# Kernel optimization log

Measured on AMD Instinct MI355X. Metric: run time of the kernel, lower is better.

The kernel has to match this reference:

```python
import math
import jax, jax.numpy as jnp
import numpy as np

D_MODEL = 2048
NUM_EXPERTS = 64
Z_LOSS_COEF = 1e-3
AUX_LOSS_COEF = 1e-2
CAPACITY_FACTOR = 1.0
MIN_CAPACITY = 4


def setup_inputs() -> dict:
    key = jax.random.key(0)
    kx, kw = jax.random.split(key)
    x = jax.random.normal(kx, (4, 4096, D_MODEL), dtype=jnp.float32)
    W = 0.02 * jax.random.normal(kw, (NUM_EXPERTS, D_MODEL), dtype=jnp.float32)  # gate weight [E, D]
    return {"x": x, "W": W}


def reference(x, W):
    B, T, D = x.shape
    N = B * T                      # num_tokens
    E = W.shape[0]
    x_flat = x.reshape(N, D)

    logits = jnp.einsum("nd,ed->ne", x_flat, W)          # gate GEMM [N, E]
    probs = jax.nn.softmax(logits, axis=-1)

    # z-loss: mean(logsumexp(logits)^2)
    z_loss = jnp.mean(jnp.square(jax.nn.logsumexp(logits, axis=-1)))

    expert_index = jnp.argmax(logits, axis=-1)            # [N] int
    expert_prob = jnp.take_along_axis(probs, expert_index[:, None], axis=-1)[:, 0]  # [N]

    counts = jnp.bincount(expert_index, length=E)         # [E] int
    f_i = counts.astype(probs.dtype) / N                  # fraction routed per expert
    p_i = jnp.mean(probs, axis=0)                         # mean router prob per expert
    aux_loss = AUX_LOSS_COEF * E * jnp.sum(f_i * p_i) + Z_LOSS_COEF * z_loss

    capacity = max(MIN_CAPACITY, math.ceil(CAPACITY_FACTOR * N / E))  # static int
    return expert_index, expert_prob, counts, capacity, aux_loss
```

## Files before the change

kernel.cpp:

```cpp
#include <hip/hip_runtime.h>
#include <math.h>

#define D_MODEL 2048
#define NE      64
#define TB      64
#define KS      2
#define KSEG    (D_MODEL / KS)
#define KC      128
#define NCH     (KSEG / KC)
#define FB_KC   32
#define FB_NCH  (D_MODEL / FB_KC)

typedef _Float16 half8 __attribute__((ext_vector_type(8)));
typedef float    f32x4 __attribute__((ext_vector_type(4)));

#define CVT1(F, HV, LV, J) do {                                               \
    float _f = (F);                                                           \
    _Float16 _h = (_Float16)_f;                                               \
    HV[J] = _h;                                                               \
    LV[J] = (_Float16)(_f - (float)_h);                                       \
} while (0)

__global__ __launch_bounds__(256) void wcvt_kernel(
    const float* __restrict__ W, short* __restrict__ Wh, short* __restrict__ Wl)
{
    const int e = blockIdx.x, t = threadIdx.x, c = t * 8;
    const float* src = W + (size_t)e * D_MODEL + c;
    float4 v0 = *(const float4*)src;
    float4 v1 = *(const float4*)(src + 4);
    half8 hv, lv;
    CVT1(v0.x * 64.0f, hv, lv, 0); CVT1(v0.y * 64.0f, hv, lv, 1);
    CVT1(v0.z * 64.0f, hv, lv, 2); CVT1(v0.w * 64.0f, hv, lv, 3);
    CVT1(v1.x * 64.0f, hv, lv, 4); CVT1(v1.y * 64.0f, hv, lv, 5);
    CVT1(v1.z * 64.0f, hv, lv, 6); CVT1(v1.w * 64.0f, hv, lv, 7);
    *(half8*)(Wh + (size_t)e * D_MODEL + c) = hv;
    *(half8*)(Wl + (size_t)e * D_MODEL + c) = lv;
}

__global__ __launch_bounds__(256, 2) void router_mfma(
    const float* __restrict__ x, const short* __restrict__ Whg,
    const short* __restrict__ Wlg, float* __restrict__ part, int ntiles)
{
    __shared__ __align__(16) char smem[65536];
    _Float16* Ah = (_Float16*)smem;
    _Float16* Al = (_Float16*)(smem + 16384);
    _Float16* Wh = (_Float16*)(smem + 32768);
    _Float16* Wl = (_Float16*)(smem + 49152);

    const int t    = threadIdx.x;
    const int tile = blockIdx.x;
    const int ks   = blockIdx.y;
    const int m0   = tile * TB;
    const int k0   = ks * KSEG;
    const int l    = t & 63;
    const int wv   = t >> 6;

    const int srow = t >> 4;
    const int sslt = t & 15;
    const int soff0 = ((sslt ^ (srow & 7)) << 3);

    float4 pa0, pa1, pa2, pa3, pa4, pa5, pa6, pa7;
    uint4  pwh0, pwh1, pwh2, pwh3, pwl0, pwl1, pwl2, pwl3;

#define PREFETCH(KB) do {                                                     \
    const float* _ap0 = x + (size_t)(m0 +  0 + srow) * D_MODEL + (KB) + sslt * 8; \
    const float* _ap1 = x + (size_t)(m0 + 16 + srow) * D_MODEL + (KB) + sslt * 8; \
    const float* _ap2 = x + (size_t)(m0 + 32 + srow) * D_MODEL + (KB) + sslt * 8; \
    const float* _ap3 = x + (size_t)(m0 + 48 + srow) * D_MODEL + (KB) + sslt * 8; \
    pa0 = *(const float4*)_ap0; pa1 = *(const float4*)(_ap0 + 4);             \
    pa2 = *(const float4*)_ap1; pa3 = *(const float4*)(_ap1 + 4);             \
    pa4 = *(const float4*)_ap2; pa5 = *(const float4*)(_ap2 + 4);             \
    pa6 = *(const float4*)_ap3; pa7 = *(const float4*)(_ap3 + 4);             \
    const size_t _w0 = (size_t)( 0 + srow) * D_MODEL + (KB) + sslt * 8;       \
    const size_t _w1 = (size_t)(16 + srow) * D_MODEL + (KB) + sslt * 8;       \
    const size_t _w2 = (size_t)(32 + srow) * D_MODEL + (KB) + sslt * 8;       \
    const size_t _w3 = (size_t)(48 + srow) * D_MODEL + (KB) + sslt * 8;       \
    pwh0 = *(const uint4*)&Whg[_w0]; pwh1 = *(const uint4*)&Whg[_w1];         \
    pwh2 = *(const uint4*)&Whg[_w2]; pwh3 = *(const uint4*)&Whg[_w3];         \
    pwl0 = *(const uint4*)&Wlg[_w0]; pwl1 = *(const uint4*)&Wlg[_w1];         \
    pwl2 = *(const uint4*)&Wlg[_w2]; pwl3 = *(const uint4*)&Wlg[_w3];         \
} while (0)

#define STORE_ITEM(I, PA, PB, PWH, PWL) do {                                  \
    half8 _hv, _lv;                                                           \
    CVT1((PA).x * 8.0f, _hv, _lv, 0); CVT1((PA).y * 8.0f, _hv, _lv, 1);       \
    CVT1((PA).z * 8.0f, _hv, _lv, 2); CVT1((PA).w * 8.0f, _hv, _lv, 3);       \
    CVT1((PB).x * 8.0f, _hv, _lv, 4); CVT1((PB).y * 8.0f, _hv, _lv, 5);       \
    CVT1((PB).z * 8.0f, _hv, _lv, 6); CVT1((PB).w * 8.0f, _hv, _lv, 7);       \
    const int _off = ((I) * 16 + srow) * 128 + soff0;                         \
    *(half8*)&Ah[_off] = _hv;                                                 \
    *(half8*)&Al[_off] = _lv;                                                 \
    *(uint4*)&Wh[_off] = PWH;                                                 \
    *(uint4*)&Wl[_off] = PWL;                                                 \
} while (0)

    PREFETCH(k0);

    f32x4 acc0 = {0.f,0.f,0.f,0.f}, acc1 = {0.f,0.f,0.f,0.f};
    f32x4 acc2 = {0.f,0.f,0.f,0.f}, acc3 = {0.f,0.f,0.f,0.f};

    for (int ch = 0; ch < NCH; ++ch) {
        __builtin_amdgcn_s_barrier();
        STORE_ITEM(0, pa0, pa1, pwh0, pwl0);
        STORE_ITEM(1, pa2, pa3, pwh1, pwl1);
        STORE_ITEM(2, pa4, pa5, pwh2, pwl2);
        STORE_ITEM(3, pa6, pa7, pwh3, pwl3);
        __builtin_amdgcn_s_barrier();
        if (ch + 1 < NCH)
            PREFETCH(k0 + (ch + 1) * KC);

        const int arow = wv * 16 + (l & 15);
        const int rsw  = l & 7;
        #pragma unroll
        for (int kq = 0; kq < 4; ++kq) {
            const int s    = kq * 4 + (l >> 4);
            const int aoff = arow * 128 + ((s ^ rsw) << 3);
            half8 ah = *(const half8*)&Ah[aoff];
            half8 al = *(const half8*)&Al[aoff];
            #pragma unroll
            for (int n = 0; n < 4; ++n) {
                const int woff = (n * 16 + (l & 15)) * 128 + ((s ^ rsw) << 3);
                half8 wh = *(const half8*)&Wh[woff];
                half8 wl = *(const half8*)&Wl[woff];
                f32x4 a = (n == 0) ? acc0 : (n == 1) ? acc1 : (n == 2) ? acc2 : acc3;
                a = __builtin_amdgcn_mfma_f32_16x16x32_f16(al, wl, a, 0, 0, 0);
                a = __builtin_amdgcn_mfma_f32_16x16x32_f16(al, wh, a, 0, 0, 0);
                a = __builtin_amdgcn_mfma_f32_16x16x32_f16(ah, wl, a, 0, 0, 0);
                a = __builtin_amdgcn_mfma_f32_16x16x32_f16(ah, wh, a, 0, 0, 0);
                if (n == 0) acc0 = a; else if (n == 1) acc1 = a;
                else if (n == 2) acc2 = a; else acc3 = a;
            }
        }
    }

    float* dst = part + ((size_t)tile * KS + ks) * (TB * NE);
    const int rbase = wv * 16 + (l >> 4) * 4;
    const int col0  = l & 15;
    #pragma unroll
    for (int q = 0; q < 4; ++q) {
        dst[(rbase + q) * NE +  0 + col0] = acc0[q] * (1.0f / 512.0f);
        dst[(rbase + q) * NE + 16 + col0] = acc1[q] * (1.0f / 512.0f);
        dst[(rbase + q) * NE + 32 + col0] = acc2[q] * (1.0f / 512.0f);
        dst[(rbase + q) * NE + 48 + col0] = acc3[q] * (1.0f / 512.0f);
    }
}

__global__ __launch_bounds__(1024) void router_stats5(
    const float* __restrict__ part, float* __restrict__ out,
    float* __restrict__ ws_prob, float* __restrict__ ws_z,
    int* __restrict__ ws_cnt, int Ntok)
{
    __shared__ float sL[64][NE + 1];
    __shared__ float red16[64][16];
    __shared__ int   arg16[64][16];
    __shared__ float smax[64], sinv[64];
    __shared__ float spart[16][NE];
    __shared__ int   hist[NE];

    const int t = threadIdx.x, b = blockIdx.x, m0 = b * 64;
    const float* base = part + (size_t)b * KS * (TB * NE);

    {
        const float* p0 = base + (size_t)t * 4;
        float s0 = 0.f, s1 = 0.f, s2 = 0.f, s3 = 0.f;
        #pragma unroll
        for (int j = 0; j < KS; ++j) {
            float4 v = *(const float4*)(p0 + (size_t)j * (TB * NE));
            s0 += v.x; s1 += v.y; s2 += v.z; s3 += v.w;
        }
        const int row = t >> 4, col = (t & 15) << 2;
        sL[row][col]     = s0; sL[row][col + 1] = s1;
        sL[row][col + 2] = s2; sL[row][col + 3] = s3;
    }
    if (t < NE) hist[t] = 0;
    __syncthreads();

    {
        const int m = t >> 4, qr = t & 15;
        float mx = -3.4e38f; int ag = qr * 4;
        #pragma unroll
        for (int k = 0; k < 4; ++k) {
            const int e = qr * 4 + k;
            float v = sL[m][e];
            if (v > mx) { mx = v; ag = e; }
        }
        red16[m][qr] = mx; arg16[m][qr] = ag;
    }
    __syncthreads();
    if (t < 64) {
        const int m = t;
        float mx = red16[m][0]; int ag = arg16[m][0];
        #pragma unroll
        for (int qr = 1; qr < 16; ++qr)
            if (red16[m][qr] > mx) { mx = red16[m][qr]; ag = arg16[m][qr]; }
        smax[m] = mx;
        out[m0 + m] = (float)ag;
        atomicAdd(&hist[ag], 1);
    }
    __syncthreads();
    {
        const int m = t >> 4, qr = t & 15;
        const float mx = smax[m];
        float s = 0.f;
        #pragma unroll
        for (int k = 0; k < 4; ++k) s += expf(sL[m][qr * 4 + k] - mx);
        red16[m][qr] = s;
    }
    __syncthreads();
    if (t < 64) {
        const int m = t;
        float s = 0.f;
        #pragma unroll
        for (int qr = 0; qr < 16; ++qr) s += red16[m][qr];
        float inv = 1.f / s;
        sinv[m] = inv;
        out[Ntok + m0 + m] = inv;
        float lse = smax[m] + logf(s);
        float z = lse * lse;
        #pragma unroll
        for (int off = 32; off > 0; off >>= 1) z += __shfl_down(z, off, 64);
        if (t == 0) ws_z[b] = z;
    }
    __syncthreads();
    {
        const int e = t & 63, g = t >> 6;
        float pa = 0.f;
        #pragma unroll
        for (int k = 0; k < 4; ++k) {
            const int m = g * 4 + k;
            pa += expf(sL[m][e] - smax[m]) * sinv[m];
        }
        spart[g][e] = pa;
    }
    __syncthreads();
    if (t < NE) {
        float ps = 0.f;
        #pragma unroll
        for (int g = 0; g < 16; ++g) ps += spart[g][t];
        ws_prob[b * NE + t] = ps;
        ws_cnt[b * NE + t]  = hist[t];
    }
}

__global__ __launch_bounds__(256) void router_final2(
    const float* __restrict__ ws_prob, const float* __restrict__ ws_z,
    const int* __restrict__ ws_cnt, float* __restrict__ out,
    int Ntok, int nblocks)
{
    __shared__ float sp[4][NE];
    __shared__ int   sc[4][NE];
    __shared__ float sz[4];

    const int e = threadIdx.x & 63, g = threadIdx.x >> 6;
    const int per = nblocks / 4;
    const int hi  = (g == 3) ? nblocks : (g + 1) * per;

    float ps = 0.f; int c = 0;
    for (int blk = g * per; blk < hi; ++blk) {
        ps += ws_prob[blk * NE + e];
        c  += ws_cnt[blk * NE + e];
    }
    sp[g][e] = ps; sc[g][e] = c;

    float z = 0.f;
    for (int blk = (int)threadIdx.x; blk < nblocks; blk += 256) z += ws_z[blk];
    #pragma unroll
    for (int off = 32; off > 0; off >>= 1) z += __shfl_down(z, off, 64);
    if (e == 0) sz[g] = z;
    __syncthreads();

    if (threadIdx.x < 64) {
        const int ee = threadIdx.x;
        float pst = ((sp[0][ee] + sp[1][ee]) + sp[2][ee]) + sp[3][ee];
        int   ct  = ((sc[0][ee] + sc[1][ee]) + sc[2][ee]) + sc[3][ee];
        out[2 * Ntok + ee] = (float)ct;

        float fN = (float)Ntok;
        float fp = ((float)ct / fN) * (pst / fN);
        #pragma unroll
        for (int off = 32; off > 0; off >>= 1) fp += __shfl_down(fp, off, 64);
        if (ee == 0) {
            float zt = ((sz[0] + sz[1]) + sz[2]) + sz[3];
            int cap = (Ntok + NE - 1) / NE;
            if (cap < 4) cap = 4;
            float aux = 0.01f * (float)NE * fp + 1e-3f * (zt / fN);
            out[2 * Ntok + NE]     = (float)cap;
            out[2 * Ntok + NE + 1] = aux;
        }
    }
}

__global__ __launch_bounds__(256) void router_main_fb(
    const float* __restrict__ x, const float* __restrict__ W,
    float* __restrict__ out, float* __restrict__ ws_prob,
    float* __restrict__ ws_z, int* __restrict__ ws_cnt, int Ntok)
{
    __shared__ __align__(16) float sX[FB_KC][68];
    __shared__ __align__(16) float sW[FB_KC][68];
    __shared__ float sL[64][65];
    __shared__ float smax[64], sinv[64];
    __shared__ float spart[4][NE];
    __shared__ int   hist[NE];

    const int t = threadIdx.x, b = blockIdx.x, m0 = b * 64;
    const int mq = t & 15, nq = t >> 4;
    const int r1 = t >> 3, r2 = r1 + 32, c1 = (t & 7) << 2;
    const float* xp1 = x + (size_t)(m0 + r1) * D_MODEL + c1;
    const float* xp2 = x + (size_t)(m0 + r2) * D_MODEL + c1;
    const float* wp1 = W + (size_t)r1 * D_MODEL + c1;
    const float* wp2 = W + (size_t)r2 * D_MODEL + c1;
    float4 ax1 = *(const float4*)xp1, ax2 = *(const float4*)xp2;
    float4 aw1 = *(const float4*)wp1, aw2 = *(const float4*)wp2;
    float a1[4][4] = {}, a2[4][4] = {};
    for (int ch = 0; ch < FB_NCH; ++ch) {
        __syncthreads();
        sX[c1+0][r1] = ax1.x; sX[c1+1][r1] = ax1.y; sX[c1+2][r1] = ax1.z; sX[c1+3][r1] = ax1.w;
        sX[c1+0][r2] = ax2.x; sX[c1+1][r2] = ax2.y; sX[c1+2][r2] = ax2.z; sX[c1+3][r2] = ax2.w;
        sW[c1+0][r1] = aw1.x; sW[c1+1][r1] = aw1.y; sW[c1+2][r1] = aw1.z; sW[c1+3][r1] = aw1.w;
        sW[c1+0][r2] = aw2.x; sW[c1+1][r2] = aw2.y; sW[c1+2][r2] = aw2.z; sW[c1+3][r2] = aw2.w;
        __syncthreads();
        if (ch + 1 < FB_NCH) {
            xp1 += FB_KC; xp2 += FB_KC; wp1 += FB_KC; wp2 += FB_KC;
            ax1 = *(const float4*)xp1; ax2 = *(const float4*)xp2;
            aw1 = *(const float4*)wp1; aw2 = *(const float4*)wp2;
        }
        #pragma unroll
        for (int k = 0; k < FB_KC; ++k) {
            float4 xa = *(const float4*)&sX[k][mq << 2];
            float4 wb = *(const float4*)&sW[k][nq << 2];
            float (*A)[4] = (k < FB_KC / 2) ? a1 : a2;
            A[0][0] = fmaf(xa.x, wb.x, A[0][0]); A[0][1] = fmaf(xa.x, wb.y, A[0][1]);
            A[0][2] = fmaf(xa.x, wb.z, A[0][2]); A[0][3] = fmaf(xa.x, wb.w, A[0][3]);
            A[1][0] = fmaf(xa.y, wb.x, A[1][0]); A[1][1] = fmaf(xa.y, wb.y, A[1][1]);
            A[1][2] = fmaf(xa.y, wb.z, A[1][2]); A[1][3] = fmaf(xa.y, wb.w, A[1][3]);
            A[2][0] = fmaf(xa.z, wb.x, A[2][0]); A[2][1] = fmaf(xa.z, wb.y, A[2][1]);
            A[2][2] = fmaf(xa.z, wb.z, A[2][2]); A[2][3] = fmaf(xa.z, wb.w, A[2][3]);
            A[3][0] = fmaf(xa.w, wb.x, A[3][0]); A[3][1] = fmaf(xa.w, wb.y, A[3][1]);
            A[3][2] = fmaf(xa.w, wb.z, A[3][2]); A[3][3] = fmaf(xa.w, wb.w, A[3][3]);
        }
    }
    #pragma unroll
    for (int i = 0; i < 4; ++i)
        #pragma unroll
        for (int j = 0; j < 4; ++j)
            sL[(mq << 2) + i][(nq << 2) + j] = a1[i][j] + a2[i][j];
    if (t < NE) hist[t] = 0;
    __syncthreads();
    if (t < 64) {
        const int m = t;
        float mx = sL[m][0]; int arg = 0;
        for (int e = 1; e < NE; ++e) { float v = sL[m][e]; if (v > mx) { mx = v; arg = e; } }
        float s = 0.f;
        for (int e = 0; e < NE; ++e) s += expf(sL[m][e] - mx);
        float inv = 1.f / s;
        out[m0 + m] = (float)arg; out[Ntok + m0 + m] = inv;
        smax[m] = mx; sinv[m] = inv;
        atomicAdd(&hist[arg], 1);
        float lse = mx + logf(s); float z = lse * lse;
        for (int off = 32; off > 0; off >>= 1) z += __shfl_down(z, off, 64);
        if (t == 0) ws_z[b] = z;
    }
    __syncthreads();
    {
        const int e = t & 63, mg = t >> 6;
        float pa = 0.f;
        for (int m = mg * 16; m < mg * 16 + 16; ++m) pa += expf(sL[m][e] - smax[m]) * sinv[m];
        spart[mg][e] = pa;
    }
    __syncthreads();
    if (t < NE) {
        ws_prob[b * NE + t] = spart[0][t] + spart[1][t] + spart[2][t] + spart[3][t];
        ws_cnt[b * NE + t]  = hist[t];
    }
}

extern "C" void kernel_launch(void* const* d_in, const int* in_sizes, int n_in,
                              void* d_out, int out_size, void* d_ws, size_t ws_size,
                              hipStream_t stream)
{
    const float* x = (const float*)d_in[0];
    const float* W = (const float*)d_in[1];
    float* out = (float*)d_out;

    const int Ntok   = in_sizes[0] / D_MODEL;
    const int ntiles = Ntok / TB;
    const int nstat  = Ntok / 64;

    const size_t wh_elems   = (size_t)NE * D_MODEL;
    const size_t part_elems = (size_t)ntiles * KS * TB * NE;
    const size_t need = wh_elems * 2 * 2
                      + (part_elems + (size_t)nstat * NE + nstat) * 4
                      + (size_t)nstat * NE * 4 + 1024;

    if ((Ntok % TB) == 0 && ws_size >= need) {
        short* wsh    = (short*)d_ws;
        short* wsl    = wsh + wh_elems;
        float* ws_part = (float*)(wsl + wh_elems);
        float* ws_prob = ws_part + part_elems;
        float* ws_z    = ws_prob + (size_t)nstat * NE;
        int*   ws_cnt  = (int*)(ws_z + nstat);

        wcvt_kernel<<<NE, 256, 0, stream>>>(W, wsh, wsl);
        dim3 grid(ntiles, KS);
        router_mfma<<<grid, 256, 0, stream>>>(x, wsh, wsl, ws_part, ntiles);
        router_stats5<<<nstat, 1024, 0, stream>>>(ws_part, out, ws_prob, ws_z, ws_cnt, Ntok);
        router_final2<<<1, 256, 0, stream>>>(ws_prob, ws_z, ws_cnt, out, Ntok, nstat);
    } else {
        const int nb = Ntok / 64;
        float* ws_prob = (float*)d_ws;
        float* ws_z    = ws_prob + (size_t)nb * NE;
        int*   ws_cnt  = (int*)(ws_z + nb);
        router_main_fb<<<nb, 256, 0, stream>>>(x, W, out, ws_prob, ws_z, ws_cnt, Ntok);
        router_final2<<<1, 256, 0, stream>>>(ws_prob, ws_z, ws_cnt, out, Ntok, nb);
    }
}
```

Baseline: 61.60 us.

## Fuse router GEMM with softmax stats and drop the K-split

Merges the MFMA gate GEMM and the per-token softmax/argmax/histogram kernel into one kernel. Each block now owns the full K range for its 64 tokens, so partial sums no longer round-trip through global memory. The x prefetch becomes double-buffered in registers, one tile ahead, to hide load latency. In exchange the grid halves (256 blocks instead of 512), which lowers parallelism across CUs, and register pressure rises from the extra prefetch buffers.

After: 64.63 us. 1.05x slower.

```diff
diff --git a/kernel.cpp b/kernel.cpp
--- a/kernel.cpp
+++ b/kernel.cpp
@@ -4,10 +4,8 @@
 #define D_MODEL 2048
 #define NE      64
 #define TB      64
-#define KS      2
-#define KSEG    (D_MODEL / KS)
 #define KC      128
-#define NCH     (KSEG / KC)
+#define NCH     (D_MODEL / KC)
 #define FB_KC   32
 #define FB_NCH  (D_MODEL / FB_KC)
 
@@ -37,40 +35,51 @@
     *(half8*)(Wl + (size_t)e * D_MODEL + c) = lv;
 }
 
-__global__ __launch_bounds__(256, 2) void router_mfma(
+__global__ __launch_bounds__(256, 2) void router_fused(
     const float* __restrict__ x, const short* __restrict__ Whg,
-    const short* __restrict__ Wlg, float* __restrict__ part, int ntiles)
+    const short* __restrict__ Wlg, float* __restrict__ out,
+    float* __restrict__ ws_prob, float* __restrict__ ws_z,
+    int* __restrict__ ws_cnt, int Ntok)
 {
     __shared__ __align__(16) char smem[65536];
     _Float16* Ah = (_Float16*)smem;
     _Float16* Al = (_Float16*)(smem + 16384);
     _Float16* Wh = (_Float16*)(smem + 32768);
     _Float16* Wl = (_Float16*)(smem + 49152);
-
-    const int t    = threadIdx.x;
-    const int tile = blockIdx.x;
-    const int ks   = blockIdx.y;
-    const int m0   = tile * TB;
-    const int k0   = ks * KSEG;
-    const int l    = t & 63;
-    const int wv   = t >> 6;
-
-    const int srow = t >> 4;
-    const int sslt = t & 15;
+    float (*sL)[NE + 1] = (float (*)[NE + 1])smem;
+    float (*red4)[4]    = (float (*)[4])(smem + 20480);
+    int   (*arg4)[4]    = (int (*)[4])(smem + 24576);
+    float* smax         = (float*)(smem + 28672);
+    float* sinv         = (float*)(smem + 28928);
+    float (*spart)[NE]  = (float (*)[NE])(smem + 29184);
+    int*   hist         = (int*)(smem + 30720);
+
+    const int t  = threadIdx.x;
+    const int b  = blockIdx.x;
+    const int m0 = b * TB;
+    const int l  = t & 63;
+    const int wv = t >> 6;
+
+    const int srow  = t >> 4;
+    const int sslt  = t & 15;
     const int soff0 = ((sslt ^ (srow & 7)) << 3);
 
-    float4 pa0, pa1, pa2, pa3, pa4, pa5, pa6, pa7;
+    float4 paA0, paA1, paA2, paA3, paA4, paA5, paA6, paA7;
+    float4 paB0, paB1, paB2, paB3, paB4, paB5, paB6, paB7;
     uint4  pwh0, pwh1, pwh2, pwh3, pwl0, pwl1, pwl2, pwl3;
 
-#define PREFETCH(KB) do {                                                     \
-    const float* _ap0 = x + (size_t)(m0 +  0 + srow) * D_MODEL + (KB) + sslt * 8; \
-    const float* _ap1 = x + (size_t)(m0 + 16 + srow) * D_MODEL + (KB) + sslt * 8; \
-    const float* _ap2 = x + (size_t)(m0 + 32 + srow) * D_MODEL + (KB) + sslt * 8; \
-    const float* _ap3 = x + (size_t)(m0 + 48 + srow) * D_MODEL + (KB) + sslt * 8; \
-    pa0 = *(const float4*)_ap0; pa1 = *(const float4*)(_ap0 + 4);             \
-    pa2 = *(const float4*)_ap1; pa3 = *(const float4*)(_ap1 + 4);             \
-    pa4 = *(const float4*)_ap2; pa5 = *(const float4*)(_ap2 + 4);             \
-    pa6 = *(const float4*)_ap3; pa7 = *(const float4*)(_ap3 + 4);             \
+#define PRE_A(P0, P1, P2, P3, P4, P5, P6, P7, KB) do {                        \
+    const float* _a0 = x + (size_t)(m0 +  0 + srow) * D_MODEL + (KB) + sslt * 8; \
+    const float* _a1 = x + (size_t)(m0 + 16 + srow) * D_MODEL + (KB) + sslt * 8; \
+    const float* _a2 = x + (size_t)(m0 + 32 + srow) * D_MODEL + (KB) + sslt * 8; \
+    const float* _a3 = x + (size_t)(m0 + 48 + srow) * D_MODEL + (KB) + sslt * 8; \
+    P0 = *(const float4*)_a0; P1 = *(const float4*)(_a0 + 4);                 \
+    P2 = *(const float4*)_a1; P3 = *(const float4*)(_a1 + 4);                 \
+    P4 = *(const float4*)_a2; P5 = *(const float4*)(_a2 + 4);                 \
+    P6 = *(const float4*)_a3; P7 = *(const float4*)(_a3 + 4);                 \
+} while (0)
+
+#define PRE_W(KB) do {                                                        \
     const size_t _w0 = (size_t)( 0 + srow) * D_MODEL + (KB) + sslt * 8;       \
     const size_t _w1 = (size_t)(16 + srow) * D_MODEL + (KB) + sslt * 8;       \
     const size_t _w2 = (size_t)(32 + srow) * D_MODEL + (KB) + sslt * 8;       \
@@ -94,124 +103,114 @@
     *(uint4*)&Wl[_off] = PWL;                                                 \
 } while (0)
 
-    PREFETCH(k0);
+#define STORE_SET(P0, P1, P2, P3, P4, P5, P6, P7) do {                        \
+    STORE_ITEM(0, P0, P1, pwh0, pwl0);                                        \
+    STORE_ITEM(1, P2, P3, pwh1, pwl1);                                        \
+    STORE_ITEM(2, P4, P5, pwh2, pwl2);                                        \
+    STORE_ITEM(3, P6, P7, pwh3, pwl3);                                        \
+} while (0)
+
+#define MFMA_PHASE() do {                                                     \
+    const int arow = wv * 16 + (l & 15);                                      \
+    const int rsw  = l & 7;                                                   \
+    _Pragma("unroll")                                                         \
+    for (int kq = 0; kq < 4; ++kq) {                                          \
+        const int s    = kq * 4 + (l >> 4);                                   \
+        const int aoff = arow * 128 + ((s ^ rsw) << 3);                       \
+        half8 ah = *(const half8*)&Ah[aoff];                                  \
+        half8 al = *(const half8*)&Al[aoff];                                  \
+        _Pragma("unroll")                                                     \
+        for (int n = 0; n < 4; ++n) {                                         \
+            const int woff = (n * 16 + (l & 15)) * 128 + ((s ^ rsw) << 3);    \
+            half8 wh = *(const half8*)&Wh[woff];                              \
+            half8 wl = *(const half8*)&Wl[woff];                              \
+            f32x4 a = (n == 0) ? acc0 : (n == 1) ? acc1 : (n == 2) ? acc2 : acc3; \
+            a = __builtin_amdgcn_mfma_f32_16x16x32_f16(al, wl, a, 0, 0, 0);   \
+            a = __builtin_amdgcn_mfma_f32_16x16x32_f16(al, wh, a, 0, 0, 0);   \
+            a = __builtin_amdgcn_mfma_f32_16x16x32_f16(ah, wl, a, 0, 0, 0);   \
+            a = __builtin_amdgcn_mfma_f32_16x16x32_f16(ah, wh, a, 0, 0, 0);   \
+            if (n == 0) acc0 = a; else if (n == 1) acc1 = a;                  \
+            else if (n == 2) acc2 = a; else acc3 = a;                         \
+        }                                                                     \
+    }                                                                         \
+} while (0)
 
     f32x4 acc0 = {0.f,0.f,0.f,0.f}, acc1 = {0.f,0.f,0.f,0.f};
     f32x4 acc2 = {0.f,0.f,0.f,0.f}, acc3 = {0.f,0.f,0.f,0.f};
 
-    for (int ch = 0; ch < NCH; ++ch) {
+    PRE_A(paA0, paA1, paA2, paA3, paA4, paA5, paA6, paA7, 0);
+    PRE_W(0);
+    PRE_A(paB0, paB1, paB2, paB3, paB4, paB5, paB6, paB7, KC);
+
+    for (int ch = 0; ch < NCH; ch += 2) {
         __builtin_amdgcn_s_barrier();
-        STORE_ITEM(0, pa0, pa1, pwh0, pwl0);
-        STORE_ITEM(1, pa2, pa3, pwh1, pwl1);
-        STORE_ITEM(2, pa4, pa5, pwh2, pwl2);
-        STORE_ITEM(3, pa6, pa7, pwh3, pwl3);
+        STORE_SET(paA0, paA1, paA2, paA3, paA4, paA5, paA6, paA7);
+        asm volatile("s_waitcnt lgkmcnt(0)" ::: "memory");
         __builtin_amdgcn_s_barrier();
-        if (ch + 1 < NCH)
-            PREFETCH(k0 + (ch + 1) * KC);
-
-        const int arow = wv * 16 + (l & 15);
-        const int rsw  = l & 7;
-        #pragma unroll
-        for (int kq = 0; kq < 4; ++kq) {
-            const int s    = kq * 4 + (l >> 4);
-            const int aoff = arow * 128 + ((s ^ rsw) << 3);
-            half8 ah = *(const half8*)&Ah[aoff];
-            half8 al = *(const half8*)&Al[aoff];
-            #pragma unroll
-            for (int n = 0; n < 4; ++n) {
-                const int woff = (n * 16 + (l & 15)) * 128 + ((s ^ rsw) << 3);
-                half8 wh = *(const half8*)&Wh[woff];
-                half8 wl = *(const half8*)&Wl[woff];
-                f32x4 a = (n == 0) ? acc0 : (n == 1) ? acc1 : (n == 2) ? acc2 : acc3;
-                a = __builtin_amdgcn_mfma_f32_16x16x32_f16(al, wl, a, 0, 0, 0);
-                a = __builtin_amdgcn_mfma_f32_16x16x32_f16(al, wh, a, 0, 0, 0);
-                a = __builtin_amdgcn_mfma_f32_16x16x32_f16(ah, wl, a, 0, 0, 0);
-                a = __builtin_amdgcn_mfma_f32_16x16x32_f16(ah, wh, a, 0, 0, 0);
-                if (n == 0) acc0 = a; else if (n == 1) acc1 = a;
-                else if (n == 2) acc2 = a; else acc3 = a;
-            }
-        }
-    }
-
-    float* dst = part + ((size_t)tile * KS + ks) * (TB * NE);
-    const int rbase = wv * 16 + (l >> 4) * 4;
-    const int col0  = l & 15;
-    #pragma unroll
-    for (int q = 0; q < 4; ++q) {
-        dst[(rbase + q) * NE +  0 + col0] = acc0[q] * (1.0f / 512.0f);
-        dst[(rbase + q) * NE + 16 + col0] = acc1[q] * (1.0f / 512.0f);
-        dst[(rbase + q) * NE + 32 + col0] = acc2[q] * (1.0f / 512.0f);
-        dst[(rbase + q) * NE + 48 + col0] = acc3[q] * (1.0f / 512.0f);
-    }
-}
-
-__global__ __launch_bounds__(1024) void router_stats5(
-    const float* __restrict__ part, float* __restrict__ out,
-    float* __restrict__ ws_prob, float* __restrict__ ws_z,
-    int* __restrict__ ws_cnt, int Ntok)
-{
-    __shared__ float sL[64][NE + 1];
-    __shared__ float red16[64][16];
-    __shared__ int   arg16[64][16];
-    __shared__ float smax[64], sinv[64];
-    __shared__ float spart[16][NE];
-    __shared__ int   hist[NE];
-
-    const int t = threadIdx.x, b = blockIdx.x, m0 = b * 64;
-    const float* base = part + (size_t)b * KS * (TB * NE);
-
+        if (ch + 1 < NCH) PRE_W((ch + 1) * KC);
+        if (ch + 2 < NCH)
+            PRE_A(paA0, paA1, paA2, paA3, paA4, paA5, paA6, paA7, (ch + 2) * KC);
+        MFMA_PHASE();
+        __builtin_amdgcn_s_barrier();
+        STORE_SET(paB0, paB1, paB2, paB3, paB4, paB5, paB6, paB7);
+        asm volatile("s_waitcnt lgkmcnt(0)" ::: "memory");
+        __builtin_amdgcn_s_barrier();
+        if (ch + 2 < NCH) PRE_W((ch + 2) * KC);
+        if (ch + 3 < NCH)
+            PRE_A(paB0, paB1, paB2, paB3, paB4, paB5, paB6, paB7, (ch + 3) * KC);
+        MFMA_PHASE();
+    }
+
+    __syncthreads();
     {
-        const float* p0 = base + (size_t)t * 4;
-        float s0 = 0.f, s1 = 0.f, s2 = 0.f, s3 = 0.f;
-        #pragma unroll
-        for (int j = 0; j < KS; ++j) {
-            float4 v = *(const float4*)(p0 + (size_t)j * (TB * NE));
-            s0 += v.x; s1 += v.y; s2 += v.z; s3 += v.w;
-        }
-        const int row = t >> 4, col = (t & 15) << 2;
-        sL[row][col]     = s0; sL[row][col + 1] = s1;
-        sL[row][col + 2] = s2; sL[row][col + 3] = s3;
+        const int rbase = wv * 16 + (l >> 4) * 4;
+        const int col0  = l & 15;
+        #pragma unroll
+        for (int q = 0; q < 4; ++q) {
+            sL[rbase + q][ 0 + col0] = acc0[q] * (1.0f / 512.0f);
+            sL[rbase + q][16 + col0] = acc1[q] * (1.0f / 512.0f);
+            sL[rbase + q][32 + col0] = acc2[q] * (1.0f / 512.0f);
+            sL[rbase + q][48 + col0] = acc3[q] * (1.0f / 512.0f);
+        }
     }
     if (t < NE) hist[t] = 0;
     __syncthreads();
 
     {
-        const int m = t >> 4, qr = t & 15;
-        float mx = -3.4e38f; int ag = qr * 4;
-        #pragma unroll
-        for (int k = 0; k < 4; ++k) {
-            const int e = qr * 4 + k;
+        const int m = t >> 2, qr = t & 3;
+        float mx = -3.4e38f; int ag = 0;
+        #pragma unroll
+        for (int k = 0; k < 16; ++k) {
+            const int e = qr * 16 + k;
             float v = sL[m][e];
             if (v > mx) { mx = v; ag = e; }
         }
-        red16[m][qr] = mx; arg16[m][qr] = ag;
+        red4[m][qr] = mx; arg4[m][qr] = ag;
     }
     __syncthreads();
     if (t < 64) {
         const int m = t;
-        float mx = red16[m][0]; int ag = arg16[m][0];
-        #pragma unroll
-        for (int qr = 1; qr < 16; ++qr)
-            if (red16[m][qr] > mx) { mx = red16[m][qr]; ag = arg16[m][qr]; }
+        float mx = red4[m][0]; int ag = arg4[m][0];
+        #pragma unroll
+        for (int qr = 1; qr < 4; ++qr)
+            if (red4[m][qr] > mx) { mx = red4[m][qr]; ag = arg4[m][qr]; }
         smax[m] = mx;
         out[m0 + m] = (float)ag;
         atomicAdd(&hist[ag], 1);
     }
     __syncthreads();
     {
-        const int m = t >> 4, qr = t & 15;
+        const int m = t >> 2, qr = t & 3;
         const float mx = smax[m];
         float s = 0.f;
         #pragma unroll
-        for (int k = 0; k < 4; ++k) s += expf(sL[m][qr * 4 + k] - mx);
-        red16[m][qr] = s;
+        for (int k = 0; k < 16; ++k) s += expf(sL[m][qr * 16 + k] - mx);
+        red4[m][qr] = s;
     }
     __syncthreads();
     if (t < 64) {
         const int m = t;
-        float s = 0.f;
-        #pragma unroll
-        for (int qr = 0; qr < 16; ++qr) s += red16[m][qr];
+        float s = ((red4[m][0] + red4[m][1]) + red4[m][2]) + red4[m][3];
         float inv = 1.f / s;
         sinv[m] = inv;
         out[Ntok + m0 + m] = inv;
@@ -223,21 +222,18 @@
     }
     __syncthreads();
     {
-        const int e = t & 63, g = t >> 6;
+        const int e = t & 63, mg = t >> 6;
         float pa = 0.f;
         #pragma unroll
-        for (int k = 0; k < 4; ++k) {
-            const int m = g * 4 + k;
+        for (int k = 0; k < 16; ++k) {
+            const int m = mg * 16 + k;
             pa += expf(sL[m][e] - smax[m]) * sinv[m];
         }
-        spart[g][e] = pa;
+        spart[mg][e] = pa;
     }
     __syncthreads();
     if (t < NE) {
-        float ps = 0.f;
-        #pragma unroll
-        for (int g = 0; g < 16; ++g) ps += spart[g][t];
-        ws_prob[b * NE + t] = ps;
+        ws_prob[b * NE + t] = ((spart[0][t] + spart[1][t]) + spart[2][t]) + spart[3][t];
         ws_cnt[b * NE + t]  = hist[t];
     }
 }
@@ -382,29 +378,25 @@
     const float* W = (const float*)d_in[1];
     float* out = (float*)d_out;
 
-    const int Ntok   = in_sizes[0] / D_MODEL;
-    const int ntiles = Ntok / TB;
-    const int nstat  = Ntok / 64;
-
-    const size_t wh_elems   = (size_t)NE * D_MODEL;
-    const size_t part_elems = (size_t)ntiles * KS * TB * NE;
+    const int Ntok = in_sizes[0] / D_MODEL;
+    const int nblk = Ntok / TB;
+
+    const size_t wh_elems = (size_t)NE * D_MODEL;
     const size_t need = wh_elems * 2 * 2
-                      + (part_elems + (size_t)nstat * NE + nstat) * 4
-                      + (size_t)nstat * NE * 4 + 1024;
-
-    if ((Ntok % TB) == 0 && ws_size >= need) {
-        short* wsh    = (short*)d_ws;
-        short* wsl    = wsh + wh_elems;
-        float* ws_part = (float*)(wsl + wh_elems);
-        float* ws_prob = ws_part + part_elems;
-        float* ws_z    = ws_prob + (size_t)nstat * NE;
-        int*   ws_cnt  = (int*)(ws_z + nstat);
+                      + ((size_t)nblk * NE + nblk) * 4
+                      + (size_t)nblk * NE * 4 + 1024;
+
+    if ((Ntok % TB) == 0 && (nblk % 4) == 0 && ws_size >= need) {
+        short* wsh     = (short*)d_ws;
+        short* wsl     = wsh + wh_elems;
+        float* ws_prob = (float*)(wsl + wh_elems);
+        float* ws_z    = ws_prob + (size_t)nblk * NE;
+        int*   ws_cnt  = (int*)(ws_z + nblk);
 
         wcvt_kernel<<<NE, 256, 0, stream>>>(W, wsh, wsl);
-        dim3 grid(ntiles, KS);
-        router_mfma<<<grid, 256, 0, stream>>>(x, wsh, wsl, ws_part, ntiles);
-        router_stats5<<<nstat, 1024, 0, stream>>>(ws_part, out, ws_prob, ws_z, ws_cnt, Ntok);
-        router_final2<<<1, 256, 0, stream>>>(ws_prob, ws_z, ws_cnt, out, Ntok, nstat);
+        router_fused<<<nblk, 256, 0, stream>>>(x, wsh, wsl, out,
+                                               ws_prob, ws_z, ws_cnt, Ntok);
+        router_final2<<<1, 256, 0, stream>>>(ws_prob, ws_z, ws_cnt, out, Ntok, nblk);
     } else {
         const int nb = Ntok / 64;
         float* ws_prob = (float*)d_ws;
```

## Load activations straight to registers and double-buffer weights in LDS

Applied to the files above, without the earlier changes.

The gate GEMM kernel is restructured so activations are loaded from global memory directly into registers in MFMA fragment layout and split into fp16 hi/lo there, instead of being staged through shared memory. Only the weight hi/lo tiles go through a double-buffered 32KB LDS region. The K chunk shrinks to 64 and each wave computes a 2x2 block of 16x16 tiles. This is meant to cut LDS traffic and barrier stalls and to overlap global loads with MFMA work, at the cost of more register pressure and less coalesced per-lane loads of x.

New measurement: 72.80 us. 18.2% more time.

```diff
diff --git a/kernel.cpp b/kernel.cpp
--- a/kernel.cpp
+++ b/kernel.cpp
@@ -4,10 +4,9 @@
 #define D_MODEL 2048
 #define NE      64
 #define TB      64
-#define KS      2
-#define KSEG    (D_MODEL / KS)
-#define KC      128
-#define NCH     (KSEG / KC)
+#define KHALF   1024
+#define KC      64
+#define NCH     (KHALF / KC)
 #define FB_KC   32
 #define FB_NCH  (D_MODEL / FB_KC)
 
@@ -37,111 +36,144 @@
     *(half8*)(Wl + (size_t)e * D_MODEL + c) = lv;
 }
 
-__global__ __launch_bounds__(256, 2) void router_mfma(
+__global__ __launch_bounds__(256, 2) void router_gemm_v4(
     const float* __restrict__ x, const short* __restrict__ Whg,
     const short* __restrict__ Wlg, float* __restrict__ part, int ntiles)
 {
-    __shared__ __align__(16) char smem[65536];
-    _Float16* Ah = (_Float16*)smem;
-    _Float16* Al = (_Float16*)(smem + 16384);
-    _Float16* Wh = (_Float16*)(smem + 32768);
-    _Float16* Wl = (_Float16*)(smem + 49152);
+    __shared__ __align__(16) char smem[32768];
 
     const int t    = threadIdx.x;
     const int tile = blockIdx.x;
     const int ks   = blockIdx.y;
     const int m0   = tile * TB;
-    const int k0   = ks * KSEG;
+    const int k0   = ks * KHALF;
     const int l    = t & 63;
     const int wv   = t >> 6;
-
-    const int srow = t >> 4;
-    const int sslt = t & 15;
-    const int soff0 = ((sslt ^ (srow & 7)) << 3);
-
-    float4 pa0, pa1, pa2, pa3, pa4, pa5, pa6, pa7;
-    uint4  pwh0, pwh1, pwh2, pwh3, pwl0, pwl1, pwl2, pwl3;
-
-#define PREFETCH(KB) do {                                                     \
-    const float* _ap0 = x + (size_t)(m0 +  0 + srow) * D_MODEL + (KB) + sslt * 8; \
-    const float* _ap1 = x + (size_t)(m0 + 16 + srow) * D_MODEL + (KB) + sslt * 8; \
-    const float* _ap2 = x + (size_t)(m0 + 32 + srow) * D_MODEL + (KB) + sslt * 8; \
-    const float* _ap3 = x + (size_t)(m0 + 48 + srow) * D_MODEL + (KB) + sslt * 8; \
-    pa0 = *(const float4*)_ap0; pa1 = *(const float4*)(_ap0 + 4);             \
-    pa2 = *(const float4*)_ap1; pa3 = *(const float4*)(_ap1 + 4);             \
-    pa4 = *(const float4*)_ap2; pa5 = *(const float4*)(_ap2 + 4);             \
-    pa6 = *(const float4*)_ap3; pa7 = *(const float4*)(_ap3 + 4);             \
-    const size_t _w0 = (size_t)( 0 + srow) * D_MODEL + (KB) + sslt * 8;       \
-    const size_t _w1 = (size_t)(16 + srow) * D_MODEL + (KB) + sslt * 8;       \
-    const size_t _w2 = (size_t)(32 + srow) * D_MODEL + (KB) + sslt * 8;       \
-    const size_t _w3 = (size_t)(48 + srow) * D_MODEL + (KB) + sslt * 8;       \
-    pwh0 = *(const uint4*)&Whg[_w0]; pwh1 = *(const uint4*)&Whg[_w1];         \
-    pwh2 = *(const uint4*)&Whg[_w2]; pwh3 = *(const uint4*)&Whg[_w3];         \
-    pwl0 = *(const uint4*)&Wlg[_w0]; pwl1 = *(const uint4*)&Wlg[_w1];         \
-    pwl2 = *(const uint4*)&Wlg[_w2]; pwl3 = *(const uint4*)&Wlg[_w3];         \
+    const int mp   = wv & 1;
+    const int np   = wv >> 1;
+
+    const int srow = t >> 2;
+    const int sc   = t & 3;
+    const int ssw  = srow & 7;
+    const int sof0 = (srow << 6) + (((sc * 2 + 0) ^ ssw) << 3);
+    const int sof1 = (srow << 6) + (((sc * 2 + 1) ^ ssw) << 3);
+    const size_t wsrc = (size_t)srow * D_MODEL + k0 + sc * 16;
+
+    const int koff = (l >> 4) * 8;
+    const float* abase0 = x + (size_t)(m0 + mp * 32 +  0 + (l & 15)) * D_MODEL + k0 + koff;
+    const float* abase1 = x + (size_t)(m0 + mp * 32 + 16 + (l & 15)) * D_MODEL + k0 + koff;
+
+    f32x4 a00 = {0.f,0.f,0.f,0.f}, a01 = {0.f,0.f,0.f,0.f};
+    f32x4 a10 = {0.f,0.f,0.f,0.f}, a11 = {0.f,0.f,0.f,0.f};
+
+    uint4  whA0, whA1, wlA0, wlA1;
+    uint4  whB0, whB1, wlB0, wlB1;
+    float4 e00, e01, e02, e03, e10, e11, e12, e13;
+    float4 o00, o01, o02, o03, o10, o11, o12, o13;
+
+#define PRE_W(WH0, WH1, WL0, WL1, CH) do {                                    \
+    const size_t _o = wsrc + (size_t)(CH) * KC;                               \
+    WH0 = *(const uint4*)&Whg[_o];     WH1 = *(const uint4*)&Whg[_o + 8];     \
+    WL0 = *(const uint4*)&Wlg[_o];     WL1 = *(const uint4*)&Wlg[_o + 8];     \
 } while (0)
 
-#define STORE_ITEM(I, PA, PB, PWH, PWL) do {                                  \
-    half8 _hv, _lv;                                                           \
-    CVT1((PA).x * 8.0f, _hv, _lv, 0); CVT1((PA).y * 8.0f, _hv, _lv, 1);       \
-    CVT1((PA).z * 8.0f, _hv, _lv, 2); CVT1((PA).w * 8.0f, _hv, _lv, 3);       \
-    CVT1((PB).x * 8.0f, _hv, _lv, 4); CVT1((PB).y * 8.0f, _hv, _lv, 5);       \
-    CVT1((PB).z * 8.0f, _hv, _lv, 6); CVT1((PB).w * 8.0f, _hv, _lv, 7);       \
-    const int _off = ((I) * 16 + srow) * 128 + soff0;                         \
-    *(half8*)&Ah[_off] = _hv;                                                 \
-    *(half8*)&Al[_off] = _lv;                                                 \
-    *(uint4*)&Wh[_off] = PWH;                                                 \
-    *(uint4*)&Wl[_off] = PWL;                                                 \
+#define STORE_W(WH0, WH1, WL0, WL1, BB) do {                                  \
+    _Float16* _Wh = (_Float16*)(smem + (BB) * 16384);                         \
+    _Float16* _Wl = (_Float16*)(smem + (BB) * 16384 + 8192);                  \
+    *(uint4*)&_Wh[sof0] = WH0;  *(uint4*)&_Wh[sof1] = WH1;                    \
+    *(uint4*)&_Wl[sof0] = WL0;  *(uint4*)&_Wl[sof1] = WL1;                    \
 } while (0)
 
-    PREFETCH(k0);
-
-    f32x4 acc0 = {0.f,0.f,0.f,0.f}, acc1 = {0.f,0.f,0.f,0.f};
-    f32x4 acc2 = {0.f,0.f,0.f,0.f}, acc3 = {0.f,0.f,0.f,0.f};
-
-    for (int ch = 0; ch < NCH; ++ch) {
+#define PRE_A(P00, P01, P02, P03, P10, P11, P12, P13, CH) do {                \
+    const float* _b0 = abase0 + (size_t)(CH) * KC;                            \
+    const float* _b1 = abase1 + (size_t)(CH) * KC;                            \
+    P00 = *(const float4*)_b0;        P01 = *(const float4*)(_b0 + 4);        \
+    P02 = *(const float4*)(_b0 + 32); P03 = *(const float4*)(_b0 + 36);       \
+    P10 = *(const float4*)_b1;        P11 = *(const float4*)(_b1 + 4);        \
+    P12 = *(const float4*)(_b1 + 32); P13 = *(const float4*)(_b1 + 36);       \
+} while (0)
+
+#define MFMA_PHASE(BB, P00, P01, P02, P03, P10, P11, P12, P13) do {           \
+    const _Float16* _Wh = (const _Float16*)(smem + (BB) * 16384);             \
+    const _Float16* _Wl = (const _Float16*)(smem + (BB) * 16384 + 8192);      \
+    _Pragma("unroll")                                                         \
+    for (int kq = 0; kq < 2; ++kq) {                                          \
+        half8 ah0, al0, ah1, al1;                                             \
+        if (kq == 0) {                                                        \
+            CVT1((P00).x * 8.0f, ah0, al0, 0); CVT1((P00).y * 8.0f, ah0, al0, 1); \
+            CVT1((P00).z * 8.0f, ah0, al0, 2); CVT1((P00).w * 8.0f, ah0, al0, 3); \
+            CVT1((P01).x * 8.0f, ah0, al0, 4); CVT1((P01).y * 8.0f, ah0, al0, 5); \
+            CVT1((P01).z * 8.0f, ah0, al0, 6); CVT1((P01).w * 8.0f, ah0, al0, 7); \
+            CVT1((P10).x * 8.0f, ah1, al1, 0); CVT1((P10).y * 8.0f, ah1, al1, 1); \
+            CVT1((P10).z * 8.0f, ah1, al1, 2); CVT1((P10).w * 8.0f, ah1, al1, 3); \
+            CVT1((P11).x * 8.0f, ah1, al1, 4); CVT1((P11).y * 8.0f, ah1, al1, 5); \
+            CVT1((P11).z * 8.0f, ah1, al1, 6); CVT1((P11).w * 8.0f, ah1, al1, 7); \
+        } else {                                                              \
+            CVT1((P02).x * 8.0f, ah0, al0, 0); CVT1((P02).y * 8.0f, ah0, al0, 1); \
+            CVT1((P02).z * 8.0f, ah0, al0, 2); CVT1((P02).w * 8.0f, ah0, al0, 3); \
+            CVT1((P03).x * 8.0f, ah0, al0, 4); CVT1((P03).y * 8.0f, ah0, al0, 5); \
+            CVT1((P03).z * 8.0f, ah0, al0, 6); CVT1((P03).w * 8.0f, ah0, al0, 7); \
+            CVT1((P12).x * 8.0f, ah1, al1, 0); CVT1((P12).y * 8.0f, ah1, al1, 1); \
+            CVT1((P12).z * 8.0f, ah1, al1, 2); CVT1((P12).w * 8.0f, ah1, al1, 3); \
+            CVT1((P13).x * 8.0f, ah1, al1, 4); CVT1((P13).y * 8.0f, ah1, al1, 5); \
+            CVT1((P13).z * 8.0f, ah1, al1, 6); CVT1((P13).w * 8.0f, ah1, al1, 7); \
+        }                                                                     \
+        const int _s = kq * 4 + (l >> 4);                                     \
+        _Pragma("unroll")                                                     \
+        for (int n = 0; n < 2; ++n) {                                         \
+            const int _row  = np * 32 + n * 16 + (l & 15);                    \
+            const int _woff = (_row << 6) + (((_s ^ (_row & 7))) << 3);       \
+            half8 _wh = *(const half8*)&_Wh[_woff];                           \
+            half8 _wl = *(const half8*)&_Wl[_woff];                           \
+            f32x4 _a = (n == 0) ? a00 : a01;                                  \
+            _a = __builtin_amdgcn_mfma_f32_16x16x32_f16(al0, _wl, _a, 0, 0, 0); \
+            _a = __builtin_amdgcn_mfma_f32_16x16x32_f16(al0, _wh, _a, 0, 0, 0); \
+            _a = __builtin_amdgcn_mfma_f32_16x16x32_f16(ah0, _wl, _a, 0, 0, 0); \
+            _a = __builtin_amdgcn_mfma_f32_16x16x32_f16(ah0, _wh, _a, 0, 0, 0); \
+            if (n == 0) a00 = _a; else a01 = _a;                              \
+            f32x4 _b = (n == 0) ? a10 : a11;                                  \
+            _b = __builtin_amdgcn_mfma_f32_16x16x32_f16(al1, _wl, _b, 0, 0, 0); \
+            _b = __builtin_amdgcn_mfma_f32_16x16x32_f16(al1, _wh, _b, 0, 0, 0); \
+            _b = __builtin_amdgcn_mfma_f32_16x16x32_f16(ah1, _wl, _b, 0, 0, 0); \
+            _b = __builtin_amdgcn_mfma_f32_16x16x32_f16(ah1, _wh, _b, 0, 0, 0); \
+            if (n == 0) a10 = _b; else a11 = _b;                              \
+        }                                                                     \
+    }                                                                         \
+} while (0)
+
+    PRE_W(whA0, whA1, wlA0, wlA1, 0);
+    STORE_W(whA0, whA1, wlA0, wlA1, 0);
+    PRE_W(whB0, whB1, wlB0, wlB1, 1);
+    PRE_A(e00, e01, e02, e03, e10, e11, e12, e13, 0);
+    PRE_A(o00, o01, o02, o03, o10, o11, o12, o13, 1);
+    asm volatile("s_waitcnt lgkmcnt(0)" ::: "memory");
+    __builtin_amdgcn_s_barrier();
+
+    for (int ch = 0; ch < NCH; ch += 2) {
+        if (ch + 1 < NCH) STORE_W(whB0, whB1, wlB0, wlB1, 1);
+        if (ch + 2 < NCH) PRE_W(whA0, whA1, wlA0, wlA1, ch + 2);
+        MFMA_PHASE(0, e00, e01, e02, e03, e10, e11, e12, e13);
+        if (ch + 2 < NCH) PRE_A(e00, e01, e02, e03, e10, e11, e12, e13, ch + 2);
+        asm volatile("s_waitcnt lgkmcnt(0)" ::: "memory");
         __builtin_amdgcn_s_barrier();
-        STORE_ITEM(0, pa0, pa1, pwh0, pwl0);
-        STORE_ITEM(1, pa2, pa3, pwh1, pwl1);
-        STORE_ITEM(2, pa4, pa5, pwh2, pwl2);
-        STORE_ITEM(3, pa6, pa7, pwh3, pwl3);
+        if (ch + 2 < NCH) STORE_W(whA0, whA1, wlA0, wlA1, 0);
+        if (ch + 3 < NCH) PRE_W(whB0, whB1, wlB0, wlB1, ch + 3);
+        MFMA_PHASE(1, o00, o01, o02, o03, o10, o11, o12, o13);
+        if (ch + 3 < NCH) PRE_A(o00, o01, o02, o03, o10, o11, o12, o13, ch + 3);
+        asm volatile("s_waitcnt lgkmcnt(0)" ::: "memory");
         __builtin_amdgcn_s_barrier();
-        if (ch + 1 < NCH)
-            PREFETCH(k0 + (ch + 1) * KC);
-
-        const int arow = wv * 16 + (l & 15);
-        const int rsw  = l & 7;
-        #pragma unroll
-        for (int kq = 0; kq < 4; ++kq) {
-            const int s    = kq * 4 + (l >> 4);
-            const int aoff = arow * 128 + ((s ^ rsw) << 3);
-            half8 ah = *(const half8*)&Ah[aoff];
-            half8 al = *(const half8*)&Al[aoff];
-            #pragma unroll
-            for (int n = 0; n < 4; ++n) {
-                const int woff = (n * 16 + (l & 15)) * 128 + ((s ^ rsw) << 3);
-                half8 wh = *(const half8*)&Wh[woff];
-                half8 wl = *(const half8*)&Wl[woff];
-                f32x4 a = (n == 0) ? acc0 : (n == 1) ? acc1 : (n == 2) ? acc2 : acc3;
-                a = __builtin_amdgcn_mfma_f32_16x16x32_f16(al, wl, a, 0, 0, 0);
-                a = __builtin_amdgcn_mfma_f32_16x16x32_f16(al, wh, a, 0, 0, 0);
-                a = __builtin_amdgcn_mfma_f32_16x16x32_f16(ah, wl, a, 0, 0, 0);
-                a = __builtin_amdgcn_mfma_f32_16x16x32_f16(ah, wh, a, 0, 0, 0);
-                if (n == 0) acc0 = a; else if (n == 1) acc1 = a;
-                else if (n == 2) acc2 = a; else acc3 = a;
-            }
-        }
-    }
-
-    float* dst = part + ((size_t)tile * KS + ks) * (TB * NE);
-    const int rbase = wv * 16 + (l >> 4) * 4;
-    const int col0  = l & 15;
+    }
+
+    float* dst = part + ((size_t)tile * 2 + ks) * (TB * NE);
+    const int q0 = (l >> 4) * 4;
+    const int c0 = np * 32 + (l & 15);
     #pragma unroll
     for (int q = 0; q < 4; ++q) {
-        dst[(rbase + q) * NE +  0 + col0] = acc0[q] * (1.0f / 512.0f);
-        dst[(rbase + q) * NE + 16 + col0] = acc1[q] * (1.0f / 512.0f);
-        dst[(rbase + q) * NE + 32 + col0] = acc2[q] * (1.0f / 512.0f);
-        dst[(rbase + q) * NE + 48 + col0] = acc3[q] * (1.0f / 512.0f);
+        const int r0 = mp * 32 + q0 + q;
+        dst[(r0) * NE + c0]           = a00[q] * (1.0f / 512.0f);
+        dst[(r0) * NE + c0 + 16]      = a01[q] * (1.0f / 512.0f);
+        dst[(r0 + 16) * NE + c0]      = a10[q] * (1.0f / 512.0f);
+        dst[(r0 + 16) * NE + c0 + 16] = a11[q] * (1.0f / 512.0f);
     }
 }
 
@@ -158,13 +190,13 @@
     __shared__ int   hist[NE];
 
     const int t = threadIdx.x, b = blockIdx.x, m0 = b * 64;
-    const float* base = part + (size_t)b * KS * (TB * NE);
+    const float* base = part + (size_t)b * 2 * (TB * NE);
 
     {
         const float* p0 = base + (size_t)t * 4;
         float s0 = 0.f, s1 = 0.f, s2 = 0.f, s3 = 0.f;
         #pragma unroll
-        for (int j = 0; j < KS; ++j) {
+        for (int j = 0; j < 2; ++j) {
             float4 v = *(const float4*)(p0 + (size_t)j * (TB * NE));
             s0 += v.x; s1 += v.y; s2 += v.z; s3 += v.w;
         }
@@ -384,27 +416,26 @@
 
     const int Ntok   = in_sizes[0] / D_MODEL;
     const int ntiles = Ntok / TB;
-    const int nstat  = Ntok / 64;
 
     const size_t wh_elems   = (size_t)NE * D_MODEL;
-    const size_t part_elems = (size_t)ntiles * KS * TB * NE;
+    const size_t part_elems = (size_t)ntiles * 2 * TB * NE;
     const size_t need = wh_elems * 2 * 2
-                      + (part_elems + (size_t)nstat * NE + nstat) * 4
-                      + (size_t)nstat * NE * 4 + 1024;
-
-    if ((Ntok % TB) == 0 && ws_size >= need) {
-        short* wsh    = (short*)d_ws;
-        short* wsl    = wsh + wh_elems;
+                      + (part_elems + (size_t)ntiles * NE + ntiles) * 4
+                      + (size_t)ntiles * NE * 4 + 1024;
+
+    if ((Ntok % TB) == 0 && (ntiles % 4) == 0 && ws_size >= need) {
+        short* wsh     = (short*)d_ws;
+        short* wsl     = wsh + wh_elems;
         float* ws_part = (float*)(wsl + wh_elems);
         float* ws_prob = ws_part + part_elems;
-        float* ws_z    = ws_prob + (size_t)nstat * NE;
-        int*   ws_cnt  = (int*)(ws_z + nstat);
+        float* ws_z    = ws_prob + (size_t)ntiles * NE;
+        int*   ws_cnt  = (int*)(ws_z + ntiles);
 
         wcvt_kernel<<<NE, 256, 0, stream>>>(W, wsh, wsl);
-        dim3 grid(ntiles, KS);
-        router_mfma<<<grid, 256, 0, stream>>>(x, wsh, wsl, ws_part, ntiles);
-        router_stats5<<<nstat, 1024, 0, stream>>>(ws_part, out, ws_prob, ws_z, ws_cnt, Ntok);
-        router_final2<<<1, 256, 0, stream>>>(ws_prob, ws_z, ws_cnt, out, Ntok, nstat);
+        dim3 grid(ntiles, 2);
+        router_gemm_v4<<<grid, 256, 0, stream>>>(x, wsh, wsl, ws_part, ntiles);
+        router_stats5<<<ntiles, 1024, 0, stream>>>(ws_part, out, ws_prob, ws_z, ws_cnt, Ntok);
+        router_final2<<<1, 256, 0, stream>>>(ws_prob, ws_z, ws_cnt, out, Ntok, ntiles);
     } else {
         const int nb = Ntok / 64;
         float* ws_prob = (float*)d_ws;
```
